# Kernel optimization log

Measured on AMD Instinct MI355X. Metric: run time of the kernel, lower is better.

Reference implementation:

```python
import jax, jax.numpy as jnp
import numpy as np

EPSILON = 0.1
ITERATIONS = 100
THRESHOLD = 0.1


def setup_inputs() -> dict:
    key = jax.random.key(0)
    kx, ky = jax.random.split(key)
    x = jax.random.normal(kx, (2048, 64), dtype=jnp.float32)
    y = jax.random.normal(ky, (2048, 64), dtype=jnp.float32)
    return {"x": x, "y": y}


def _sinkhorn(x, y):
    N, M = x.shape[0], y.shape[0]
    # l2 ground metric: C[i,j] = sum_d (x[i,d] - y[j,d])^2   -> [N, M]
    C = jnp.sum((x[:, None, :] - y[None, :, :]) ** 2, axis=-1)
    log_a = jnp.log(1.0 / N + 1e-8)  # uniform marginals (scalar broadcast)
    log_b = jnp.log(1.0 / M + 1e-8)

    def kernel(u, v):
        # log Boltzmann kernel: (-C + u_i + v_j) / epsilon
        return (-C + u[:, None] + v[None, :]) / EPSILON

    def step(carry, _):
        u, v, done = carry
        K = kernel(u, v)
        u_new = EPSILON * (log_a - jax.nn.logsumexp(K, axis=1)) + u
        K2 = kernel(u_new, v)
        # torch: logsumexp(K2.T, dim=1) == logsumexp(K2, axis=0)
        v_new = EPSILON * (log_b - jax.nn.logsumexp(K2, axis=0)) + v
        diff = jnp.sum(jnp.abs(u_new - u)) + jnp.sum(jnp.abs(v_new - v))
        # emulate the host-side early break: freeze state once converged
        u_out = jnp.where(done, u, u_new)
        v_out = jnp.where(done, v, v_new)
        done = done | (diff < THRESHOLD)
        return (u_out, v_out, done), None

    init = (jnp.zeros((N,), C.dtype), jnp.zeros((M,), C.dtype),
            jnp.asarray(False))
    (u, v, _), _ = jax.lax.scan(step, init, None, length=ITERATIONS)

    pi = jnp.exp(kernel(u, v))          # transport plan [N, M]
    cost = jnp.sum(pi * C)              # scalar OT cost
    return cost, pi


def reference(x, y):
    return _sinkhorn(x, y)
```

## Files before the change

### kernel.cpp

```cpp
#include <hip/hip_runtime.h>
#include <cstddef>

static constexpr int   NN      = 2048;
static constexpr int   TPB_B   = 256;
static constexpr int   TPB     = 1024;
static constexpr int   NWB     = TPB / 64;
static constexpr int   NB      = 128;
static constexpr int   MAX_IT  = 100;
static constexpr float EPS     = 0.1f;
static constexpr float INV_EPS = 10.0f;
static constexpr float LOG_AB  = -7.6245985063594f;
static constexpr float THRESH  = 0.1f;

#define ALOAD(p)     __hip_atomic_load((p),  __ATOMIC_RELAXED, __HIP_MEMORY_SCOPE_AGENT)
#define ASTORE(p, x) __hip_atomic_store((p), (x), __ATOMIC_RELAXED, __HIP_MEMORY_SCOPE_AGENT)

typedef unsigned long long u64;

__global__ __launch_bounds__(TPB_B)
void build_cost(const float* __restrict__ x, const float* __restrict__ y,
                float* __restrict__ C, float* __restrict__ CT,
                unsigned* __restrict__ zz, int zcount,
                int c_aligned, int use_ct)
{
    __shared__ float xs[64][65];
    __shared__ float ys[64][65];
    const int t  = threadIdx.x;
    const int bi = blockIdx.y, bj = blockIdx.x;

    if (bi == 0) {
        int per = (zcount + 31) / 32;
        int lo = bj * per;
        int hi = lo + per; if (hi > zcount) hi = zcount;
        for (int idx = lo + t; idx < hi; idx += TPB_B) zz[idx] = 0u;
    }

#pragma unroll
    for (int k = 0; k < 16; ++k) {
        int idx = t + TPB_B * k;
        int r = idx >> 6, c = idx & 63;
        xs[r][c] = x[(size_t)(bi * 64 + r) * 64 + c];
        ys[r][c] = y[(size_t)(bj * 64 + r) * 64 + c];
    }
    __syncthreads();

    const int ti0 = (t >> 4) * 4;
    const int tj0 = (t & 15) * 4;
    float acc[4][4] = {};
#pragma unroll 8
    for (int d = 0; d < 64; ++d) {
        float xv[4], yv[4];
#pragma unroll
        for (int k = 0; k < 4; ++k) xv[k] = xs[ti0 + k][d];
#pragma unroll
        for (int l = 0; l < 4; ++l) yv[l] = ys[tj0 + l][d];
#pragma unroll
        for (int k = 0; k < 4; ++k)
#pragma unroll
            for (int l = 0; l < 4; ++l) {
                float df = xv[k] - yv[l];
                acc[k][l] = fmaf(df, df, acc[k][l]);
            }
    }

#pragma unroll
    for (int k = 0; k < 4; ++k) {
        size_t off = (size_t)(bi * 64 + ti0 + k) * NN + bj * 64 + tj0;
        if (c_aligned) {
            *(float4*)(C + off) = make_float4(acc[k][0], acc[k][1], acc[k][2], acc[k][3]);
        } else {
            C[off + 0] = acc[k][0]; C[off + 1] = acc[k][1];
            C[off + 2] = acc[k][2]; C[off + 3] = acc[k][3];
        }
    }
    if (use_ct) {
#pragma unroll
        for (int l = 0; l < 4; ++l) {
            size_t off = (size_t)(bj * 64 + tj0 + l) * NN + bi * 64 + ti0;
            *(float4*)(CT + off) = make_float4(acc[0][l], acc[1][l], acc[2][l], acc[3][l]);
        }
    }
}

__device__ __forceinline__ void load_row32(const float* row, int lane,
                                           int aligned, float c[32])
{
    if (aligned) {
        const float4* r4 = (const float4*)row;
#pragma unroll
        for (int k = 0; k < 8; ++k) {
            float4 A = r4[lane + 64 * k];
            c[4*k+0] = A.x; c[4*k+1] = A.y; c[4*k+2] = A.z; c[4*k+3] = A.w;
        }
    } else {
#pragma unroll
        for (int k = 0; k < 8; ++k) {
            const float* p = row + 4 * (lane + 64 * k);
            c[4*k+0] = p[0]; c[4*k+1] = p[1]; c[4*k+2] = p[2]; c[4*k+3] = p[3];
        }
    }
}

__device__ __forceinline__ void lds_row32(const float* sv, int lane, float b[32])
{
    const float4* s4 = (const float4*)sv;
#pragma unroll
    for (int k = 0; k < 8; ++k) {
        float4 A = s4[lane + 64 * k];
        b[4*k+0] = A.x; b[4*k+1] = A.y; b[4*k+2] = A.z; b[4*k+3] = A.w;
    }
}

__device__ __forceinline__ float wave_lse(const float c[32], const float b[32])
{
    float M = b[0] - c[0];
#pragma unroll
    for (int k = 1; k < 32; ++k) M = fmaxf(M, b[k] - c[k]);
#pragma unroll
    for (int off = 1; off < 64; off <<= 1) M = fmaxf(M, __shfl_xor(M, off));
    float Ms = M * INV_EPS;
    float s = 0.0f;
#pragma unroll
    for (int k = 0; k < 32; ++k) s += __expf(fmaf(b[k] - c[k], INV_EPS, -Ms));
#pragma unroll
    for (int off = 1; off < 64; off <<= 1) s += __shfl_xor(s, off);
    return Ms + __logf(s);
}

__global__ __launch_bounds__(TPB)
void sinkhorn_main(const float* Cm, const float* __restrict__ CT,
                   u64* __restrict__ valA, u64* __restrict__ valB,
                   u64* __restrict__ rotR, u64* __restrict__ rotC,
                   u64* __restrict__ costb,
                   float* out, int c_aligned, int use_ct)
{
    __shared__ float sv[2048];
    __shared__ float swave[NWB];
    __shared__ float sdw[NWB];
    __shared__ float sred4[4];
    __shared__ float sdiff;
    const int t = threadIdx.x, lane = t & 63, w = t >> 6, b = blockIdx.x;
    const int i = b * NWB + w;

    float crow[32], ccol[32];
    load_row32(Cm + (size_t)i * NN, lane, c_aligned, crow);
    if (use_ct) {
        load_row32(CT + (size_t)i * NN, lane, 1, ccol);
    } else {
#pragma unroll
        for (int k = 0; k < 8; ++k)
#pragma unroll
            for (int kk = 0; kk < 4; ++kk)
                ccol[4*k+kk] = Cm[(size_t)(4 * (lane + 64 * k) + kk) * NN + i];
    }

    for (int k = t; k < 2048; k += TPB) sv[k] = 0.0f;
    __syncthreads();

    float u_keep = 0.0f, v_keep = 0.0f;
    float b32[32];

    for (int it = 0; it < MAX_IT; ++it) {
        const unsigned ep = (unsigned)(it + 1);

        lds_row32(sv, lane, b32);
        float lse   = wave_lse(crow, b32);
        float u_new = EPS * (LOG_AB - lse);
        float pdr   = fabsf(u_new - u_keep);

        if (it >= 1) {
            if (t < NB) {
                u64 r1, r2;
                const int ri = (it & 3) * NB + t;
                for (;;) { r1 = ALOAD(&rotR[ri]);
                           if ((unsigned)(r1 >> 32) >= (unsigned)it) break; }
                for (;;) { r2 = ALOAD(&rotC[ri]);
                           if ((unsigned)(r2 >> 32) >= (unsigned)it) break; }
                float d = __uint_as_float((unsigned)r1) +
                          __uint_as_float((unsigned)r2);
#pragma unroll
                for (int off = 1; off < 64; off <<= 1) d += __shfl_xor(d, off);
                if (lane == 0) sred4[w] = d;
            }
            __syncthreads();
            if (t == 0) sdiff = sred4[0] + sred4[1];
            __syncthreads();
            if (sdiff < THRESH) break;
        }
        u_keep = u_new;

        if (lane == 0) { swave[w] = u_new; sdw[w] = pdr; }
        __syncthreads();
        if (t < NWB)
            ASTORE(&valA[b * NWB + t],
                   ((u64)ep << 32) | __float_as_uint(swave[t]));
        if (t == 0) {
            float ps = 0.0f;
#pragma unroll
            for (int k = 0; k < NWB; ++k) ps += sdw[k];
            ASTORE(&rotR[(ep & 3) * NB + b],
                   ((u64)ep << 32) | __float_as_uint(ps));
        }
        {
            const int base = 2 * t;
            u64 d0, d1;
            for (;;) {
                d0 = ALOAD(&valA[base + 0]);
                d1 = ALOAD(&valA[base + 1]);
                if (((unsigned)(d0 >> 32) >= ep) & ((unsigned)(d1 >> 32) >= ep))
                    break;
            }
            ((float2*)sv)[t] = make_float2(__uint_as_float((unsigned)d0),
                                           __uint_as_float((unsigned)d1));
        }
        __syncthreads();

        lds_row32(sv, lane, b32);
        lse = wave_lse(ccol, b32);
        float v_new = EPS * (LOG_AB - lse);
        float pdc   = fabsf(v_new - v_keep);
        v_keep = v_new;

        if (lane == 0) { swave[w] = v_new; sdw[w] = pdc; }
        __syncthreads();
        if (t < NWB)
            ASTORE(&valB[b * NWB + t],
                   ((u64)ep << 32) | __float_as_uint(swave[t]));
        if (t == 0) {
            float ps = 0.0f;
#pragma unroll
            for (int k = 0; k < NWB; ++k) ps += sdw[k];
            ASTORE(&rotC[(ep & 3) * NB + b],
                   ((u64)ep << 32) | __float_as_uint(ps));
        }
        {
            const int base = 2 * t;
            u64 d0, d1;
            for (;;) {
                d0 = ALOAD(&valB[base + 0]);
                d1 = ALOAD(&valB[base + 1]);
                if (((unsigned)(d0 >> 32) >= ep) & ((unsigned)(d1 >> 32) >= ep))
                    break;
            }
            ((float2*)sv)[t] = make_float2(__uint_as_float((unsigned)d0),
                                           __uint_as_float((unsigned)d1));
        }
        __syncthreads();
    }

    float cpart = 0.0f;
    {
        lds_row32(sv, lane, b32);
        const float ui = u_keep;
        float* orow = out + 1 + (size_t)i * NN;
#pragma unroll
        for (int k = 0; k < 8; ++k) {
#pragma unroll
            for (int kk = 0; kk < 4; ++kk) {
                float cc = crow[4*k+kk];
                float p  = __expf((ui + b32[4*k+kk] - cc) * INV_EPS);
                cpart = fmaf(p, cc, cpart);
                orow[4 * (lane + 64 * k) + kk] = p;
            }
        }
    }
#pragma unroll
    for (int off = 1; off < 64; off <<= 1) cpart += __shfl_xor(cpart, off);
    if (lane == 0) sdw[w] = cpart;
    __syncthreads();
    if (t == 0) {
        float pc = 0.0f;
#pragma unroll
        for (int k = 0; k < NWB; ++k) pc += sdw[k];
        ASTORE(&costb[b], (1ull << 32) | __float_as_uint(pc));
    }
    if (b == 0) {
        if (t < NB) {
            u64 h;
            for (;;) { h = ALOAD(&costb[t]); if (h >= (1ull << 32)) break; }
            float pc = __uint_as_float((unsigned)h);
#pragma unroll
            for (int off = 1; off < 64; off <<= 1) pc += __shfl_xor(pc, off);
            if (lane == 0) sred4[w] = pc;
        }
        __syncthreads();
        if (t == 0) out[0] = sred4[0] + sred4[1];
    }
}

extern "C" void kernel_launch(void* const* d_in, const int* in_sizes, int n_in,
                              void* d_out, int out_size, void* d_ws, size_t ws_size,
                              hipStream_t stream)
{
    (void)in_sizes; (void)n_in; (void)out_size;
    const float* x = (const float*)d_in[0];
    const float* y = (const float*)d_in[1];
    float* out = (float*)d_out;
    char*  ws  = (char*)d_ws;

    const size_t CB = (size_t)NN * NN * sizeof(float);
    const int    ZU = 2048 + 2048 + 512 + 512 + 128;
    const size_t ZB = (size_t)ZU * sizeof(u64);

    float *Cm, *CT; char* zz;
    int c_aligned, use_ct;
    if (ws_size >= 2 * CB + ZB) {
        Cm = (float*)ws; CT = (float*)(ws + CB); zz = ws + 2 * CB;
        c_aligned = 1; use_ct = 1;
    } else if (ws_size >= CB + ZB) {
        Cm = out + 1; CT = (float*)ws; zz = ws + CB;
        c_aligned = 0; use_ct = 1;
    } else {
        Cm = out + 1; CT = nullptr; zz = ws;
        c_aligned = 0; use_ct = 0;
    }
    u64* valA  = (u64*)zz;
    u64* valB  = valA + 2048;
    u64* rotR  = valB + 2048;
    u64* rotC  = rotR + 512;
    u64* costb = rotC + 512;
    int  zcount = ZU * 2;

    hipLaunchKernelGGL(build_cost, dim3(32, 32), dim3(TPB_B), 0, stream,
                       x, y, Cm, CT, (unsigned*)zz, zcount, c_aligned, use_ct);

    const float* Cmc = Cm;
    const float* CTc = CT;
    void* args[] = { (void*)&Cmc, (void*)&CTc, (void*)&valA, (void*)&valB,
                     (void*)&rotR, (void*)&rotC, (void*)&costb,
                     (void*)&out, (void*)&c_aligned, (void*)&use_ct };
    hipLaunchCooperativeKernel((void*)sinkhorn_main, dim3(NB), dim3(TPB),
                               args, 0, stream);
}
```

Before: 737.6 us.

## Compute convergence diff redundantly per block and drop cross-block diff exchange

```diff
diff --git a/kernel.cpp b/kernel.cpp
--- a/kernel.cpp
+++ b/kernel.cpp
@@ -130,15 +130,13 @@
 __global__ __launch_bounds__(TPB)
 void sinkhorn_main(const float* Cm, const float* __restrict__ CT,
                    u64* __restrict__ valA, u64* __restrict__ valB,
-                   u64* __restrict__ rotR, u64* __restrict__ rotC,
                    u64* __restrict__ costb,
                    float* out, int c_aligned, int use_ct)
 {
-    __shared__ float sv[2048];
-    __shared__ float swave[NWB];
-    __shared__ float sdw[NWB];
-    __shared__ float sred4[4];
-    __shared__ float sdiff;
+    __shared__ __align__(16) float svA[2048];
+    __shared__ __align__(16) float svB[2048];
+    __shared__ float sdu[2][NWB];
+    __shared__ float sdv[2][NWB];
     const int t = threadIdx.x, lane = t & 63, w = t >> 6, b = blockIdx.x;
     const int i = b * NWB + w;
 
@@ -154,55 +152,33 @@
                 ccol[4*k+kk] = Cm[(size_t)(4 * (lane + 64 * k) + kk) * NN + i];
     }
 
-    for (int k = t; k < 2048; k += TPB) sv[k] = 0.0f;
+    for (int k = t; k < 2048; k += TPB) svB[k] = 0.0f;
     __syncthreads();
 
-    float u_keep = 0.0f, v_keep = 0.0f;
+    float u_keep = 0.0f;
+    float uo0 = 0.0f, uo1 = 0.0f, vo0 = 0.0f, vo1 = 0.0f;
     float b32[32];
+    const int base = 2 * t;
 
     for (int it = 0; it < MAX_IT; ++it) {
         const unsigned ep = (unsigned)(it + 1);
 
-        lds_row32(sv, lane, b32);
+        if (it >= 1) {
+            const int pp = (it - 1) & 1;
+            float sd = 0.0f;
+#pragma unroll
+            for (int k = 0; k < NWB; ++k) sd += sdu[pp][k] + sdv[pp][k];
+            if (sd < THRESH) break;
+        }
+
+        lds_row32(svB, lane, b32);
         float lse   = wave_lse(crow, b32);
         float u_new = EPS * (LOG_AB - lse);
-        float pdr   = fabsf(u_new - u_keep);
-
-        if (it >= 1) {
-            if (t < NB) {
-                u64 r1, r2;
-                const int ri = (it & 3) * NB + t;
-                for (;;) { r1 = ALOAD(&rotR[ri]);
-                           if ((unsigned)(r1 >> 32) >= (unsigned)it) break; }
-                for (;;) { r2 = ALOAD(&rotC[ri]);
-                           if ((unsigned)(r2 >> 32) >= (unsigned)it) break; }
-                float d = __uint_as_float((unsigned)r1) +
-                          __uint_as_float((unsigned)r2);
-#pragma unroll
-                for (int off = 1; off < 64; off <<= 1) d += __shfl_xor(d, off);
-                if (lane == 0) sred4[w] = d;
-            }
-            __syncthreads();
-            if (t == 0) sdiff = sred4[0] + sred4[1];
-            __syncthreads();
-            if (sdiff < THRESH) break;
-        }
+        if (lane == 0)
+            ASTORE(&valA[i], ((u64)ep << 32) | __float_as_uint(u_new));
         u_keep = u_new;
 
-        if (lane == 0) { swave[w] = u_new; sdw[w] = pdr; }
-        __syncthreads();
-        if (t < NWB)
-            ASTORE(&valA[b * NWB + t],
-                   ((u64)ep << 32) | __float_as_uint(swave[t]));
-        if (t == 0) {
-            float ps = 0.0f;
-#pragma unroll
-            for (int k = 0; k < NWB; ++k) ps += sdw[k];
-            ASTORE(&rotR[(ep & 3) * NB + b],
-                   ((u64)ep << 32) | __float_as_uint(ps));
-        }
         {
-            const int base = 2 * t;
             u64 d0, d1;
             for (;;) {
                 d0 = ALOAD(&valA[base + 0]);
@@ -210,31 +186,24 @@
                 if (((unsigned)(d0 >> 32) >= ep) & ((unsigned)(d1 >> 32) >= ep))
                     break;
             }
-            ((float2*)sv)[t] = make_float2(__uint_as_float((unsigned)d0),
-                                           __uint_as_float((unsigned)d1));
+            float f0 = __uint_as_float((unsigned)d0);
+            float f1 = __uint_as_float((unsigned)d1);
+            ((float2*)svA)[t] = make_float2(f0, f1);
+            float d = fabsf(f0 - uo0) + fabsf(f1 - uo1);
+            uo0 = f0; uo1 = f1;
+#pragma unroll
+            for (int off = 1; off < 64; off <<= 1) d += __shfl_xor(d, off);
+            if (lane == 0) sdu[it & 1][w] = d;
         }
         __syncthreads();
 
-        lds_row32(sv, lane, b32);
+        lds_row32(svA, lane, b32);
         lse = wave_lse(ccol, b32);
         float v_new = EPS * (LOG_AB - lse);
-        float pdc   = fabsf(v_new - v_keep);
-        v_keep = v_new;
-
-        if (lane == 0) { swave[w] = v_new; sdw[w] = pdc; }
-        __syncthreads();
-        if (t < NWB)
-            ASTORE(&valB[b * NWB + t],
-                   ((u64)ep << 32) | __float_as_uint(swave[t]));
-        if (t == 0) {
-            float ps = 0.0f;
-#pragma unroll
-            for (int k = 0; k < NWB; ++k) ps += sdw[k];
-            ASTORE(&rotC[(ep & 3) * NB + b],
-                   ((u64)ep << 32) | __float_as_uint(ps));
-        }
+        if (lane == 0)
+            ASTORE(&valB[i], ((u64)ep << 32) | __float_as_uint(v_new));
+
         {
-            const int base = 2 * t;
             u64 d0, d1;
             for (;;) {
                 d0 = ALOAD(&valB[base + 0]);
@@ -242,15 +211,21 @@
                 if (((unsigned)(d0 >> 32) >= ep) & ((unsigned)(d1 >> 32) >= ep))
                     break;
             }
-            ((float2*)sv)[t] = make_float2(__uint_as_float((unsigned)d0),
-                                           __uint_as_float((unsigned)d1));
+            float f0 = __uint_as_float((unsigned)d0);
+            float f1 = __uint_as_float((unsigned)d1);
+            ((float2*)svB)[t] = make_float2(f0, f1);
+            float d = fabsf(f0 - vo0) + fabsf(f1 - vo1);
+            vo0 = f0; vo1 = f1;
+#pragma unroll
+            for (int off = 1; off < 64; off <<= 1) d += __shfl_xor(d, off);
+            if (lane == 0) sdv[it & 1][w] = d;
         }
         __syncthreads();
     }
 
     float cpart = 0.0f;
     {
-        lds_row32(sv, lane, b32);
+        lds_row32(svB, lane, b32);
         const float ui = u_keep;
         float* orow = out + 1 + (size_t)i * NN;
 #pragma unroll
@@ -266,12 +241,12 @@
     }
 #pragma unroll
     for (int off = 1; off < 64; off <<= 1) cpart += __shfl_xor(cpart, off);
-    if (lane == 0) sdw[w] = cpart;
+    if (lane == 0) sdu[0][w] = cpart;
     __syncthreads();
     if (t == 0) {
         float pc = 0.0f;
 #pragma unroll
-        for (int k = 0; k < NWB; ++k) pc += sdw[k];
+        for (int k = 0; k < NWB; ++k) pc += sdu[0][k];
         ASTORE(&costb[b], (1ull << 32) | __float_as_uint(pc));
     }
     if (b == 0) {
@@ -281,10 +256,10 @@
             float pc = __uint_as_float((unsigned)h);
 #pragma unroll
             for (int off = 1; off < 64; off <<= 1) pc += __shfl_xor(pc, off);
-            if (lane == 0) sred4[w] = pc;
+            if (lane == 0) sdv[0][w] = pc;
         }
         __syncthreads();
-        if (t == 0) out[0] = sred4[0] + sred4[1];
+        if (t == 0) out[0] = sdv[0][0] + sdv[0][1];
     }
 }
 
@@ -299,7 +274,7 @@
     char*  ws  = (char*)d_ws;
 
     const size_t CB = (size_t)NN * NN * sizeof(float);
-    const int    ZU = 2048 + 2048 + 512 + 512 + 128;
+    const int    ZU = 2048 + 2048 + 128;
     const size_t ZB = (size_t)ZU * sizeof(u64);
 
     float *Cm, *CT; char* zz;
@@ -316,9 +291,7 @@
     }
     u64* valA  = (u64*)zz;
     u64* valB  = valA + 2048;
-    u64* rotR  = valB + 2048;
-    u64* rotC  = rotR + 512;
-    u64* costb = rotC + 512;
+    u64* costb = valB + 2048;
     int  zcount = ZU * 2;
 
     hipLaunchKernelGGL(build_cost, dim3(32, 32), dim3(TPB_B), 0, stream,
@@ -327,8 +300,8 @@
     const float* Cmc = Cm;
     const float* CTc = CT;
     void* args[] = { (void*)&Cmc, (void*)&CTc, (void*)&valA, (void*)&valB,
-                     (void*)&rotR, (void*)&rotC, (void*)&costb,
-                     (void*)&out, (void*)&c_aligned, (void*)&use_ct };
+                     (void*)&costb, (void*)&out, (void*)&c_aligned,
+                     (void*)&use_ct };
     hipLaunchCooperativeKernel((void*)sinkhorn_main, dim3(NB), dim3(TPB),
                                args, 0, stream);
 }
```

Measured after the change: 1.589 ms. 2.15x slower.
